# Kernel optimization log

Measured on AMD Instinct MI355X. Metric: run time of the kernel, lower is better.

## Reference

```python
import jax, jax.numpy as jnp
import numpy as np
from jax import lax

B, N, NPOINT, NSAMPLE = 16, 8192, 1024, 32
RADIUS = 0.2
EPS = 1e-5


def setup_inputs() -> dict:
    key = jax.random.key(0)
    ks = jax.random.split(key, 6)
    return {
        "xyz": jax.random.uniform(ks[0], (B, N, 3), dtype=jnp.float32),
        "points": jax.random.normal(ks[1], (B, N, 64), dtype=jnp.float32),
        "w1": jax.random.normal(ks[2], (64, 67), dtype=jnp.float32) * 0.1,
        "b1": jnp.zeros((64,), jnp.float32),
        "g1": jnp.ones((64,), jnp.float32),
        "be1": jnp.zeros((64,), jnp.float32),
        "w2": jax.random.normal(ks[3], (64, 64), dtype=jnp.float32) * 0.1,
        "b2": jnp.zeros((64,), jnp.float32),
        "g2": jnp.ones((64,), jnp.float32),
        "be2": jnp.zeros((64,), jnp.float32),
        "w3": jax.random.normal(ks[4], (128, 64), dtype=jnp.float32) * 0.1,
        "b3": jnp.zeros((128,), jnp.float32),
        "g3": jnp.ones((128,), jnp.float32),
        "be3": jnp.zeros((128,), jnp.float32),
    }


def farthest_point_sample(xyz, npoint):
    # Sequential FPS; deterministic start at index 0 (torch uses a random start).
    b, n, _ = xyz.shape
    batch_ix = jnp.arange(b)

    def step(carry, _):
        distance, farthest = carry
        centroid = xyz[batch_ix, farthest]              # [B,3]
        dist = jnp.sum((xyz - centroid[:, None, :]) ** 2, -1)  # [B,N]
        distance = jnp.minimum(distance, dist)
        return (distance, jnp.argmax(distance, -1).astype(jnp.int32)), farthest

    init = (jnp.full((b, n), 1e10, jnp.float32), jnp.zeros((b,), jnp.int32))
    _, idxs = lax.scan(step, init, None, length=npoint)
    return idxs.T                                        # [B,npoint]


def gather_points(points, idx):
    # points [B,N,C], idx [B,...] -> [B,...,C]
    return jax.vmap(lambda p, i: p[i])(points, idx)


def query_ball_point(radius, nsample, xyz, new_xyz):
    b, n, _ = xyz.shape
    sqrd = jnp.sum((new_xyz[:, :, None, :] - xyz[:, None, :, :]) ** 2, -1)  # [B,S,N]
    gidx = jnp.where(sqrd > radius ** 2, n, jnp.arange(n, dtype=jnp.int32)[None, None, :])
    gidx = jnp.sort(gidx, axis=-1)[:, :, :nsample]       # [B,S,K]
    first = gidx[:, :, :1]
    return jnp.where(gidx == n, first, gidx)


def conv_bn_relu(x, w, b, g, be):
    # x [B,C,S,K]; 1x1 conv == channel matmul, then train-mode BN over (B,S,K).
    y = jnp.einsum("bcsk,oc->bosk", x, w) + b[None, :, None, None]
    mean = jnp.mean(y, axis=(0, 2, 3), keepdims=True)
    var = jnp.mean((y - mean) ** 2, axis=(0, 2, 3), keepdims=True)
    yhat = (y - mean) * lax.rsqrt(var + EPS)
    return jax.nn.relu(yhat * g[None, :, None, None] + be[None, :, None, None])


def reference(xyz, points, w1, b1, g1, be1, w2, b2, g2, be2, w3, b3, g3, be3):
    fps_idx = farthest_point_sample(xyz, NPOINT)          # [B,S]
    new_xyz = gather_points(xyz, fps_idx)                 # [B,S,3]
    idx = query_ball_point(RADIUS, NSAMPLE, xyz, new_xyz) # [B,S,K]
    grouped_xyz = gather_points(xyz, idx)                 # [B,S,K,3]
    grouped_xyz_norm = grouped_xyz - new_xyz[:, :, None, :]
    grouped_points = gather_points(points, idx)           # [B,S,K,64]
    new_points = jnp.concatenate([grouped_xyz_norm, grouped_points], axis=-1)
    x = jnp.transpose(new_points, (0, 3, 1, 2))           # [B,67,S,K]
    x = conv_bn_relu(x, w1, b1, g1, be1)
    x = conv_bn_relu(x, w2, b2, g2, be2)
    x = conv_bn_relu(x, w3, b3, g3, be3)
    new_points_out = jnp.max(x, axis=-1)                  # [B,128,S]
    return new_xyz, new_points_out
```

## Files before the change

kernel.cpp:

```cpp
#include <hip/hip_runtime.h>
#include <hip/hip_bf16.h>

typedef unsigned short u16;
typedef unsigned long long u64;
typedef __attribute__((ext_vector_type(8))) short short8;
typedef __attribute__((ext_vector_type(4))) float f32x4;

#define NN 8192
#define SSAMP 1024
#define KK 32
#define NT_F 524288.0f
#define EPSV 1e-5f

__device__ __forceinline__ u64 umax64(u64 a, u64 b) { return a > b ? a : b; }

template <int C>
__device__ __forceinline__ void dppstep(unsigned& hi, unsigned& lo) {
  unsigned h2 = (unsigned)__builtin_amdgcn_update_dpp(0, (int)hi, C, 0xF, 0xF, true);
  unsigned l2 = (unsigned)__builtin_amdgcn_update_dpp(0, (int)lo, C, 0xF, 0xF, true);
  u64 a = ((u64)hi << 32) | lo;
  u64 b = ((u64)h2 << 32) | l2;
  bool g = b > a;
  hi = g ? h2 : hi;
  lo = g ? l2 : lo;
}

__device__ __forceinline__ u64 wave_max_key(u64 key) {
  unsigned hi = (unsigned)(key >> 32), lo = (unsigned)key;
  dppstep<0x111>(hi, lo);
  dppstep<0x112>(hi, lo);
  dppstep<0x114>(hi, lo);
  dppstep<0x118>(hi, lo);
  dppstep<0x142>(hi, lo);
  dppstep<0x143>(hi, lo);
  return ((u64)hi << 32) | lo;
}

__device__ __forceinline__ int morton3(int ix, int iy, int iz) {
  int m = (((ix >> 0) & 1) << 2) | (((iy >> 0) & 1) << 1) | (((iz >> 0) & 1) << 0);
  m |= (((ix >> 1) & 1) << 5) | (((iy >> 1) & 1) << 4) | (((iz >> 1) & 1) << 3);
  m |= (((ix >> 2) & 1) << 8) | (((iy >> 2) & 1) << 7) | (((iz >> 2) & 1) << 6);
  return m;
}

__global__ __launch_bounds__(1024, 1) void fps_bucket_kernel(const float* __restrict__ xyz,
                                                             float* __restrict__ newxyz) {
  extern __shared__ float dynls[];
  float* sx = dynls;
  float* sy = dynls + NN;
  float* sz = dynls + 2 * NN;
  int* sI = (int*)(dynls + 3 * NN);
  __shared__ int cnt[512], off[512];
  __shared__ u64 candS[3];
  __shared__ int pos0_sh;

  const int b = blockIdx.x, t = threadIdx.x;
  const float* base = xyz + (size_t)b * NN * 3;

  float px[8], py[8], pz[8];
  int pc[8];
  if (t < 512) cnt[t] = 0;
  if (t == 0) { candS[0] = 0; candS[1] = 0; candS[2] = 0; }
  __syncthreads();
#pragma unroll
  for (int j = 0; j < 8; j++) {
    int p = j * 1024 + t;
    px[j] = base[p * 3 + 0];
    py[j] = base[p * 3 + 1];
    pz[j] = base[p * 3 + 2];
    int ix = min(7, (int)(px[j] * 8.0f));
    int iy = min(7, (int)(py[j] * 8.0f));
    int iz = min(7, (int)(pz[j] * 8.0f));
    pc[j] = morton3(ix, iy, iz);
    atomicAdd(&cnt[pc[j]], 1);
  }
  __syncthreads();
  int myc = (t < 512) ? cnt[t] : 0;
  for (int st = 1; st < 512; st <<= 1) {
    int v = 0;
    if (t < 512) { v = cnt[t]; if (t >= st) v += cnt[t - st]; }
    __syncthreads();
    if (t < 512) cnt[t] = v;
    __syncthreads();
  }
  if (t < 512) off[t] = cnt[t] - myc;
  __syncthreads();
#pragma unroll
  for (int j = 0; j < 8; j++) {
    int pos = atomicAdd(&off[pc[j]], 1);
    sx[pos] = px[j]; sy[pos] = py[j]; sz[pos] = pz[j];
    int orig = j * 1024 + t;
    sI[pos] = orig;
    if (orig == 0) pos0_sh = pos;
  }
  __syncthreads();
  float X[8], Y[8], Z[8], D[8];
  unsigned L26[8];
  float lox = 1e30f, loy = 1e30f, loz = 1e30f;
  float hix = -1e30f, hiy = -1e30f, hiz = -1e30f;
#pragma unroll
  for (int j = 0; j < 8; j++) {
    int p = t * 8 + j;
    float x = sx[p], y = sy[p], z = sz[p];
    X[j] = x; Y[j] = y; Z[j] = z; D[j] = 1e10f;
    int orig = sI[p];
    L26[j] = ((unsigned)(8191 - orig) << 13) | (unsigned)p;
    lox = fminf(lox, x); hix = fmaxf(hix, x);
    loy = fminf(loy, y); hiy = fmaxf(hiy, y);
    loz = fminf(loz, z); hiz = fmaxf(hiz, z);
  }
  int cur = pos0_sh;
  u64 ckey = 0;
  float cbd = 1e30f;
  u64 wkeyS = 0;
  int s = 0;

  for (int it = 0; it < SSAMP; it++) {
    const int sn = (s == 2) ? 0 : s + 1;
    float cx = sx[cur], cy = sy[cur], cz = sz[cur];
    if (t == 0) {
      float* o = newxyz + ((size_t)b * SSAMP + it) * 3;
      o[0] = cx; o[1] = cy; o[2] = cz;
    }
    float ddx = fmaxf(fmaxf(lox - cx, cx - hix), 0.f);
    float ddy = fmaxf(fmaxf(loy - cy, cy - hiy), 0.f);
    float ddz = fmaxf(fmaxf(loz - cz, cz - hiz), 0.f);
    float lb2 = fmaf(ddx, ddx, fmaf(ddy, ddy, ddz * ddz));
    bool upd = lb2 <= fmaf(cbd, 1.0001f, 1e-12f);
    if (__ballot(upd)) {
      if (upd) {
        u64 k = 0;
        float bd = -1.0f;
#pragma unroll
        for (int j = 0; j < 8; j++) {
          float dx = __fsub_rn(X[j], cx);
          float dy = __fsub_rn(Y[j], cy);
          float dz = __fsub_rn(Z[j], cz);
          float d = __fadd_rn(__fadd_rn(__fmul_rn(dx, dx), __fmul_rn(dy, dy)), __fmul_rn(dz, dz));
          float dm = fminf(D[j], d);
          D[j] = dm;
          bd = fmaxf(bd, dm);
          u64 kj = ((u64)__float_as_uint(dm) << 26) | (u64)L26[j];
          k = umax64(k, kj);
        }
        ckey = k;
        cbd = bd;
      }
      wkeyS = wave_max_key(ckey);
    }
    if ((t & 63) == 63) atomicMax(&candS[s], wkeyS);
    if (t == 0) candS[sn] = 0;
    __syncthreads();
    cur = (int)(candS[s] & 0x1FFFull);
    s = sn;
  }
}

__global__ __launch_bounds__(512, 1) void fps_fallback_kernel(const float* __restrict__ xyz,
                                                              float* __restrict__ newxyz) {
  const int b = blockIdx.x, t = threadIdx.x;
  const float* base = xyz + (size_t)b * NN * 3;
  __shared__ u64 cand[2][8];
  float X[16], Y[16], Z[16], D[16];
#pragma unroll
  for (int j = 0; j < 16; j++) {
    int p = j * 512 + t;
    X[j] = base[p * 3 + 0];
    Y[j] = base[p * 3 + 1];
    Z[j] = base[p * 3 + 2];
    D[j] = 1e10f;
  }
  __syncthreads();
  int cur = 0;
  const int w = t >> 6;
  for (int it = 0; it < SSAMP; it++) {
    float cx = base[cur * 3 + 0];
    float cy = base[cur * 3 + 1];
    float cz = base[cur * 3 + 2];
    if (t == 0) {
      float* o = newxyz + ((size_t)b * SSAMP + it) * 3;
      o[0] = cx; o[1] = cy; o[2] = cz;
    }
    float bestd = -1.0f;
    int bj = 0;
#pragma unroll
    for (int j = 0; j < 16; j++) {
      float dx = __fsub_rn(X[j], cx);
      float dy = __fsub_rn(Y[j], cy);
      float dz = __fsub_rn(Z[j], cz);
      float d = __fadd_rn(__fadd_rn(__fmul_rn(dx, dx), __fmul_rn(dy, dy)), __fmul_rn(dz, dz));
      float dm = fminf(D[j], d);
      D[j] = dm;
      bool g = dm > bestd;
      bestd = g ? dm : bestd;
      bj = g ? j : bj;
    }
    u64 key = ((u64)__float_as_uint(bestd) << 32) |
              (u64)(unsigned)~(unsigned)(bj * 512 + t);
    key = wave_max_key(key);
    const int s = it & 1;
    if ((t & 63) == 63) cand[s][w] = key;
    __syncthreads();
    u64 c0 = cand[s][0], c1 = cand[s][1], c2 = cand[s][2], c3 = cand[s][3];
    u64 c4 = cand[s][4], c5 = cand[s][5], c6 = cand[s][6], c7 = cand[s][7];
    u64 a0 = umax64(c0, c1), a1 = umax64(c2, c3), a2 = umax64(c4, c5), a3 = umax64(c6, c7);
    u64 best = umax64(umax64(a0, a1), umax64(a2, a3));
    cur = (int)(~(unsigned)(best & 0xFFFFFFFFull));
  }
}

__global__ __launch_bounds__(256) void ballq_kernel(const float* __restrict__ xyz,
                                                    const float* __restrict__ newxyz,
                                                    int* __restrict__ ballidx) {
  const int wid = blockIdx.x * 4 + (threadIdx.x >> 6);
  const int lane = threadIdx.x & 63;
  const int b = wid >> 10;
  const float* base = xyz + (size_t)b * NN * 3;
  const float cx = newxyz[wid * 3 + 0];
  const float cy = newxyz[wid * 3 + 1];
  const float cz = newxyz[wid * 3 + 2];
  int* op = ballidx + (size_t)wid * KK;
  int cnt = 0, first = -1;
  for (int p0 = 0; p0 < NN; p0 += 64) {
    const int p = p0 + lane;
    float dx = __fsub_rn(cx, base[p * 3 + 0]);
    float dy = __fsub_rn(cy, base[p * 3 + 1]);
    float dz = __fsub_rn(cz, base[p * 3 + 2]);
    float d = __fadd_rn(__fadd_rn(__fmul_rn(dx, dx), __fmul_rn(dy, dy)), __fmul_rn(dz, dz));
    bool hit = d <= 0.04f;
    u64 m = __ballot(hit);
    if (m) {
      if (first < 0) first = p0 + __ffsll((long long)m) - 1;
      int rank = __popcll(m & ((1ull << lane) - 1ull));
      int slot = cnt + rank;
      if (hit && slot < KK) op[slot] = p;
      cnt += __popcll(m);
      if (cnt >= KK) break;
    }
  }
  if (cnt < KK && lane >= cnt && lane < KK) op[lane] = first;
}

__global__ __launch_bounds__(256) void collapse_kernel(const float* __restrict__ bkt,
                                                       float* __restrict__ dst) {
  int e = blockIdx.x * 256 + threadIdx.x;
  float s = 0.f;
#pragma unroll 8
  for (int u = 0; u < 64; u++) s += bkt[u * 512 + e];
  dst[e] = s;
}

__device__ __forceinline__ void put2(short8& r, int x, float f0, float f1) {
  __hip_bfloat162 p = __float22bfloat162_rn(make_float2(f0, f1));
  unsigned u = *(const unsigned*)&p;
  r[x] = (short)(u16)(u & 0xFFFF);
  r[x + 1] = (short)(u16)(u >> 16);
}

__device__ __forceinline__ short8 bn_pack8(const u16 h[8], const float* sS, const float* sT, int c0) {
  short8 r;
#pragma unroll
  for (int x = 0; x < 8; x += 2) {
    float f0 = __bfloat162float(*(const __hip_bfloat16*)&h[x]);
    float f1 = __bfloat162float(*(const __hip_bfloat16*)&h[x + 1]);
    f0 = fmaxf(fmaf(f0, sS[c0 + x], sT[c0 + x]), 0.f);
    f1 = fmaxf(fmaf(f1, sS[c0 + x + 1], sT[c0 + x + 1]), 0.f);
    put2(r, x, f0, f1);
  }
  return r;
}

__device__ __forceinline__ short8 w_pack8(const float v[8]) {
  short8 r;
#pragma unroll
  for (int x = 0; x < 8; x += 2) put2(r, x, v[x], v[x + 1]);
  return r;
}

__global__ __launch_bounds__(256) void gemm1_mfma_kernel(const float* __restrict__ xyz,
                                                         const float* __restrict__ pts,
                                                         const float* __restrict__ w1,
                                                         const float* __restrict__ b1,
                                                         const float* __restrict__ newxyz,
                                                         const int* __restrict__ ballidx,
                                                         u16* __restrict__ Y,
                                                         float* __restrict__ bkt) {
  __shared__ __align__(16) short Af[12 * 64 * 8];
  __shared__ __align__(16) short Bf[12 * 64 * 8];
  __shared__ __align__(16) u16 Cs[64 * 72];
  __shared__ int sidx[64];
  __shared__ float snx[6];
  __shared__ float sSum[64], sSq[64];
  const int t = threadIdx.x, blk = blockIdx.x;
  const int pbase = blk * 64;
  const int g0 = pbase >> 5;
  const int b = g0 >> 10;
  if (t < 64) sidx[t] = ballidx[pbase + t];
  if (t < 6) snx[t] = newxyz[(size_t)g0 * 3 + t];
  __syncthreads();
  {
    int r = t >> 2, q = t & 3;
    const float4* prow = (const float4*)(pts + ((size_t)b * NN + sidx[r]) * 64);
    float4 v0 = prow[q * 4 + 0], v1 = prow[q * 4 + 1];
    float4 v2 = prow[q * 4 + 2], v3 = prow[q * 4 + 3];
    float f0[8] = {v0.x, v0.y, v0.z, v0.w, v1.x, v1.y, v1.z, v1.w};
    float f1[8] = {v2.x, v2.y, v2.z, v2.w, v3.x, v3.y, v3.z, v3.w};
    int kt = q >> 1, mt = r >> 4, m = r & 15;
    int qp0 = (2 * q) & 3, qp1 = (2 * q + 1) & 3;
    *(short8*)&Af[((mt * 3 + kt) * 64 + qp0 * 16 + m) * 8] = w_pack8(f0);
    *(short8*)&Af[((mt * 3 + kt) * 64 + qp1 * 16 + m) * 8] = w_pack8(f1);
  }
  {
    int o = t >> 2, q = t & 3;
    const float* wr = w1 + o * 67 + 3 + q * 16;
    float f0[8], f1[8];
#pragma unroll
    for (int x = 0; x < 8; x++) { f0[x] = wr[x]; f1[x] = wr[8 + x]; }
    int kt = q >> 1, nt = o >> 4, n = o & 15;
    int qp0 = (2 * q) & 3, qp1 = (2 * q + 1) & 3;
    *(short8*)&Bf[((nt * 3 + kt) * 64 + qp0 * 16 + n) * 8] = w_pack8(f0);
    *(short8*)&Bf[((nt * 3 + kt) * 64 + qp1 * 16 + n) * 8] = w_pack8(f1);
  }
  if (t < 64) {
    const float* xp = xyz + ((size_t)b * NN + sidx[t]) * 3;
    int g = t >> 5, mt = t >> 4, m = t & 15;
    float xn = xp[0] - snx[g * 3 + 0];
    float yn = xp[1] - snx[g * 3 + 1];
    float zn = xp[2] - snx[g * 3 + 2];
    short8 s0 = {0, 0, 0, 0, 0, 0, 0, 0};
    short8 z8 = {0, 0, 0, 0, 0, 0, 0, 0};
    __hip_bfloat16 hb;
    hb = __float2bfloat16(xn); s0[0] = *(const short*)&hb;
    hb = __float2bfloat16(yn); s0[1] = *(const short*)&hb;
    hb = __float2bfloat16(zn); s0[2] = *(const short*)&hb;
    *(short8*)&Af[((mt * 3 + 2) * 64 + 0 * 16 + m) * 8] = s0;
    *(short8*)&Af[((mt * 3 + 2) * 64 + 1 * 16 + m) * 8] = z8;
    *(short8*)&Af[((mt * 3 + 2) * 64 + 2 * 16 + m) * 8] = z8;
    *(short8*)&Af[((mt * 3 + 2) * 64 + 3 * 16 + m) * 8] = z8;
  } else if (t < 128) {
    int o = t - 64, nt = o >> 4, n = o & 15;
    short8 s0 = {0, 0, 0, 0, 0, 0, 0, 0};
    short8 z8 = {0, 0, 0, 0, 0, 0, 0, 0};
    __hip_bfloat16 hb;
    hb = __float2bfloat16(w1[o * 67 + 0]); s0[0] = *(const short*)&hb;
    hb = __float2bfloat16(w1[o * 67 + 1]); s0[1] = *(const short*)&hb;
    hb = __float2bfloat16(w1[o * 67 + 2]); s0[2] = *(const short*)&hb;
    *(short8*)&Bf[((nt * 3 + 2) * 64 + 0 * 16 + n) * 8] = s0;
    *(short8*)&Bf[((nt * 3 + 2) * 64 + 1 * 16 + n) * 8] = z8;
    *(short8*)&Bf[((nt * 3 + 2) * 64 + 2 * 16 + n) * 8] = z8;
    *(short8*)&Bf[((nt * 3 + 2) * 64 + 3 * 16 + n) * 8] = z8;
  }
  __syncthreads();
  const int w = t >> 6, L = t & 63, q = L >> 4;
  const int nt = w;
  short8 b0 = *(const short8*)&Bf[((nt * 3 + 0) * 64 + L) * 8];
  short8 b1v = *(const short8*)&Bf[((nt * 3 + 1) * 64 + L) * 8];
  short8 b2v = *(const short8*)&Bf[((nt * 3 + 2) * 64 + L) * 8];
  const int o = nt * 16 + (L & 15);
  const float bl = b1[o];
  f32x4 acc[4];
#pragma unroll
  for (int mt = 0; mt < 4; mt++) {
    acc[mt] = (f32x4){0.f, 0.f, 0.f, 0.f};
    short8 a0 = *(const short8*)&Af[((mt * 3 + 0) * 64 + L) * 8];
    short8 a1 = *(const short8*)&Af[((mt * 3 + 1) * 64 + L) * 8];
    short8 a2 = *(const short8*)&Af[((mt * 3 + 2) * 64 + L) * 8];
    acc[mt] = __builtin_amdgcn_mfma_f32_16x16x32_bf16(a0, b0, acc[mt], 0, 0, 0);
    acc[mt] = __builtin_amdgcn_mfma_f32_16x16x32_bf16(a1, b1v, acc[mt], 0, 0, 0);
    acc[mt] = __builtin_amdgcn_mfma_f32_16x16x32_bf16(a2, b2v, acc[mt], 0, 0, 0);
  }
  float s = 0.f, q2 = 0.f;
#pragma unroll
  for (int mt = 0; mt < 4; mt++) {
    float yv[4];
#pragma unroll
    for (int r = 0; r < 4; r++) {
      yv[r] = acc[mt][r] + bl;
      s += yv[r]; q2 += yv[r] * yv[r];
    }
#pragma unroll
    for (int r = 0; r < 4; r += 2) {
      __hip_bfloat162 p = __float22bfloat162_rn(make_float2(yv[r], yv[r + 1]));
      unsigned u = *(const unsigned*)&p;
      Cs[(mt * 16 + q * 4 + r) * 72 + o] = (u16)(u & 0xFFFF);
      Cs[(mt * 16 + q * 4 + r + 1) * 72 + o] = (u16)(u >> 16);
    }
  }
  s += __shfl_xor(s, 16); s += __shfl_xor(s, 32);
  q2 += __shfl_xor(q2, 16); q2 += __shfl_xor(q2, 32);
  if (L < 16) { sSum[o] = s; sSq[o] = q2; }
  __syncthreads();
  {
    int r = t >> 2, qq = t & 3;
    uint4 c0 = *(const uint4*)&Cs[r * 72 + qq * 16];
    uint4 c1 = *(const uint4*)&Cs[r * 72 + qq * 16 + 8];
    uint4* yrow = (uint4*)(Y + (size_t)(pbase + r) * 64);
    yrow[qq * 2] = c0; yrow[qq * 2 + 1] = c1;
  }
  float* bb = bkt + (size_t)(blk & 63) * 512;
  if (t < 64) atomicAdd(&bb[t], sSum[t]);
  else if (t < 128) atomicAdd(&bb[64 + (t - 64)], sSq[t - 64]);
}

__global__ __launch_bounds__(256) void gemm2_mfma_kernel(u16* __restrict__ Y,
                                                         const float* __restrict__ w2,
                                                         const float* __restrict__ b2,
                                                         const float* __restrict__ g1,
                                                         const float* __restrict__ be1,
                                                         const float* __restrict__ statsC,
                                                         float* __restrict__ bkt) {
  __shared__ __align__(16) short Af[8 * 64 * 8];
  __shared__ __align__(16) short Bf[8 * 64 * 8];
  __shared__ __align__(16) u16 Cs[64 * 72];
  __shared__ float sS[64], sT[64];
  __shared__ float sSum[64], sSq[64];
  const int t = threadIdx.x, blk = blockIdx.x;
  const int pbase = blk * 64;
  if (t < 64) {
    float mean = statsC[t] * (1.0f / NT_F);
    float var = statsC[64 + t] * (1.0f / NT_F) - mean * mean;
    float s = g1[t] * rsqrtf(var + EPSV);
    sS[t] = s;
    sT[t] = be1[t] - mean * s;
  }
  __syncthreads();
  {
    int r = t >> 2, q = t & 3;
    const uint4* yrow = (const uint4*)(Y + (size_t)(pbase + r) * 64);
    union { uint4 u; u16 h[8]; } v0, v1;
    v0.u = yrow[q * 2]; v1.u = yrow[q * 2 + 1];
    int c0 = q * 16;
    int kt = c0 >> 5, mt = r >> 4;
    int qp0 = (c0 >> 3) & 3, qp1 = ((c0 + 8) >> 3) & 3;
    *(short8*)&Af[(((mt << 1) | kt) * 64 + qp0 * 16 + (r & 15)) * 8] = bn_pack8(v0.h, sS, sT, c0);
    *(short8*)&Af[(((mt << 1) | kt) * 64 + qp1 * 16 + (r & 15)) * 8] = bn_pack8(v1.h, sS, sT, c0 + 8);
  }
  {
    int o = t >> 2, q = t & 3;
    const float* wrow = w2 + o * 64 + q * 16;
    float f0[8], f1[8];
#pragma unroll
    for (int x = 0; x < 8; x++) { f0[x] = wrow[x]; f1[x] = wrow[8 + x]; }
    int c0 = q * 16;
    int kt = c0 >> 5, nt = o >> 4;
    int qp0 = (c0 >> 3) & 3, qp1 = ((c0 + 8) >> 3) & 3;
    *(short8*)&Bf[(((nt << 1) | kt) * 64 + qp0 * 16 + (o & 15)) * 8] = w_pack8(f0);
    *(short8*)&Bf[(((nt << 1) | kt) * 64 + qp1 * 16 + (o & 15)) * 8] = w_pack8(f1);
  }
  __syncthreads();
  const int w = t >> 6, L = t & 63, q = L >> 4;
  const int nt = w;
  short8 b0 = *(const short8*)&Bf[((nt * 2 + 0) * 64 + L) * 8];
  short8 b1 = *(const short8*)&Bf[((nt * 2 + 1) * 64 + L) * 8];
  const int o = nt * 16 + (L & 15);
  const float bl = b2[o];
  f32x4 acc[4];
#pragma unroll
  for (int mt = 0; mt < 4; mt++) {
    acc[mt] = (f32x4){0.f, 0.f, 0.f, 0.f};
    short8 a0 = *(const short8*)&Af[((mt * 2 + 0) * 64 + L) * 8];
    short8 a1 = *(const short8*)&Af[((mt * 2 + 1) * 64 + L) * 8];
    acc[mt] = __builtin_amdgcn_mfma_f32_16x16x32_bf16(a0, b0, acc[mt], 0, 0, 0);
    acc[mt] = __builtin_amdgcn_mfma_f32_16x16x32_bf16(a1, b1, acc[mt], 0, 0, 0);
  }
  float s = 0.f, q2 = 0.f;
#pragma unroll
  for (int mt = 0; mt < 4; mt++) {
    float yv[4];
#pragma unroll
    for (int r = 0; r < 4; r++) {
      yv[r] = acc[mt][r] + bl;
      s += yv[r]; q2 += yv[r] * yv[r];
    }
#pragma unroll
    for (int r = 0; r < 4; r += 2) {
      __hip_bfloat162 p = __float22bfloat162_rn(make_float2(yv[r], yv[r + 1]));
      unsigned u = *(const unsigned*)&p;
      Cs[(mt * 16 + q * 4 + r) * 72 + o] = (u16)(u & 0xFFFF);
      Cs[(mt * 16 + q * 4 + r + 1) * 72 + o] = (u16)(u >> 16);
    }
  }
  s += __shfl_xor(s, 16); s += __shfl_xor(s, 32);
  q2 += __shfl_xor(q2, 16); q2 += __shfl_xor(q2, 32);
  if (L < 16) { sSum[o] = s; sSq[o] = q2; }
  __syncthreads();
  {
    int r = t >> 2, qq = t & 3;
    uint4 c0 = *(const uint4*)&Cs[r * 72 + qq * 16];
    uint4 c1 = *(const uint4*)&Cs[r * 72 + qq * 16 + 8];
    uint4* yrow = (uint4*)(Y + (size_t)(pbase + r) * 64);
    yrow[qq * 2] = c0; yrow[qq * 2 + 1] = c1;
  }
  float* bb = bkt + (size_t)(blk & 63) * 512;
  if (t < 64) atomicAdd(&bb[128 + t], sSum[t]);
  else if (t < 128) atomicAdd(&bb[192 + (t - 64)], sSq[t - 64]);
}

__global__ __launch_bounds__(256) void conv3max_mfma_kernel(const u16* __restrict__ Y,
                                                            const float* __restrict__ w3,
                                                            const float* __restrict__ b3,
                                                            const float* __restrict__ g2,
                                                            const float* __restrict__ be2,
                                                            const float* __restrict__ statsC,
                                                            float* __restrict__ bkt,
                                                            float* __restrict__ gmax,
                                                            float* __restrict__ gmin) {
  __shared__ __align__(16) short Af[8 * 64 * 8];
  __shared__ __align__(16) short Bf[16 * 64 * 8];
  __shared__ float sS[64], sT[64];
  __shared__ float sSum[128], sSq[128];
  const int t = threadIdx.x, blk = blockIdx.x;
  const int pbase = blk * 64;
  if (t < 64) {
    float mean = statsC[128 + t] * (1.0f / NT_F);
    float var = statsC[192 + t] * (1.0f / NT_F) - mean * mean;
    float s = g2[t] * rsqrtf(var + EPSV);
    sS[t] = s;
    sT[t] = be2[t] - mean * s;
  }
  __syncthreads();
  {
    int r = t >> 2, q = t & 3;
    const uint4* yrow = (const uint4*)(Y + (size_t)(pbase + r) * 64);
    union { uint4 u; u16 h[8]; } v0, v1;
    v0.u = yrow[q * 2]; v1.u = yrow[q * 2 + 1];
    int c0 = q * 16;
    int kt = c0 >> 5, mt = r >> 4;
    int qp0 = (c0 >> 3) & 3, qp1 = ((c0 + 8) >> 3) & 3;
    *(short8*)&Af[(((mt << 1) | kt) * 64 + qp0 * 16 + (r & 15)) * 8] = bn_pack8(v0.h, sS, sT, c0);
    *(short8*)&Af[(((mt << 1) | kt) * 64 + qp1 * 16 + (r & 15)) * 8] = bn_pack8(v1.h, sS, sT, c0 + 8);
  }
  {
    int o = t >> 1, h = t & 1;
    const float* wrow = w3 + o * 64 + h * 32;
    int nt = o >> 4;
#pragma unroll
    for (int g = 0; g < 4; g++) {
      float f[8];
#pragma unroll
      for (int x = 0; x < 8; x++) f[x] = wrow[g * 8 + x];
      *(short8*)&Bf[(((nt << 1) | h) * 64 + g * 16 + (o & 15)) * 8] = w_pack8(f);
    }
  }
  __syncthreads();
  const int w = t >> 6, L = t & 63, q = L >> 4;
  f32x4 acc[2][4];
#pragma unroll
  for (int n = 0; n < 2; n++)
#pragma unroll
    for (int mt = 0; mt < 4; mt++) acc[n][mt] = (f32x4){0.f, 0.f, 0.f, 0.f};
  short8 bfr[2][2];
#pragma unroll
  for (int n = 0; n < 2; n++) {
    int nt = 2 * w + n;
    bfr[n][0] = *(const short8*)&Bf[((nt * 2 + 0) * 64 + L) * 8];
    bfr[n][1] = *(const short8*)&Bf[((nt * 2 + 1) * 64 + L) * 8];
  }
#pragma unroll
  for (int mt = 0; mt < 4; mt++) {
    short8 a0 = *(const short8*)&Af[((mt * 2 + 0) * 64 + L) * 8];
    short8 a1 = *(const short8*)&Af[((mt * 2 + 1) * 64 + L) * 8];
#pragma unroll
    for (int n = 0; n < 2; n++) {
      acc[n][mt] = __builtin_amdgcn_mfma_f32_16x16x32_bf16(a0, bfr[n][0], acc[n][mt], 0, 0, 0);
      acc[n][mt] = __builtin_amdgcn_mfma_f32_16x16x32_bf16(a1, bfr[n][1], acc[n][mt], 0, 0, 0);
    }
  }
#pragma unroll
  for (int n = 0; n < 2; n++) {
    int o = (2 * w + n) * 16 + (L & 15);
    float bl = b3[o];
    float s = 0.f, q2 = 0.f;
    float gmx[2] = {-1e30f, -1e30f}, gmn[2] = {1e30f, 1e30f};
#pragma unroll
    for (int mt = 0; mt < 4; mt++) {
      int g = mt >> 1;
#pragma unroll
      for (int r = 0; r < 4; r++) {
        float y = acc[n][mt][r] + bl;
        s += y; q2 += y * y;
        gmx[g] = fmaxf(gmx[g], y);
        gmn[g] = fminf(gmn[g], y);
      }
    }
    s += __shfl_xor(s, 16); s += __shfl_xor(s, 32);
    q2 += __shfl_xor(q2, 16); q2 += __shfl_xor(q2, 32);
#pragma unroll
    for (int g = 0; g < 2; g++) {
      gmx[g] = fmaxf(gmx[g], __shfl_xor(gmx[g], 16));
      gmx[g] = fmaxf(gmx[g], __shfl_xor(gmx[g], 32));
      gmn[g] = fminf(gmn[g], __shfl_xor(gmn[g], 16));
      gmn[g] = fminf(gmn[g], __shfl_xor(gmn[g], 32));
    }
    if (L < 16) {
      sSum[o] = s; sSq[o] = q2;
#pragma unroll
      for (int g = 0; g < 2; g++) {
        gmax[(size_t)(blk * 2 + g) * 128 + o] = gmx[g];
        gmin[(size_t)(blk * 2 + g) * 128 + o] = gmn[g];
      }
    }
  }
  __syncthreads();
  float* bb = bkt + (size_t)(blk & 63) * 512;
  if (t < 128) atomicAdd(&bb[256 + t], sSum[t]);
  else atomicAdd(&bb[384 + (t - 128)], sSq[t - 128]);
}

__global__ __launch_bounds__(256) void finalize_kernel(const float* __restrict__ gmax,
                                                       const float* __restrict__ gmin,
                                                       const float* __restrict__ statsC,
                                                       const float* __restrict__ g3,
                                                       const float* __restrict__ be3,
                                                       float* __restrict__ outf) {
  __shared__ float smax[64 * 65], smin[64 * 65];
  __shared__ float ssc[64], ssh[64];
  const int t = threadIdx.x, blk = blockIdx.x;
  const int b = blk >> 5, st = (blk >> 1) & 15, oh = blk & 1;
  const int o0 = oh * 64, g0 = b * 1024 + st * 64;
  if (t < 64) {
    int o = o0 + t;
    float mean = statsC[256 + o] * (1.0f / NT_F);
    float var = statsC[384 + o] * (1.0f / NT_F) - mean * mean;
    float sc = g3[o] * rsqrtf(var + EPSV);
    ssc[t] = sc;
    ssh[t] = be3[o] - mean * sc;
  }
  const int col = t & 63, rw = t >> 6;
#pragma unroll
  for (int k = 0; k < 16; k++) {
    int r = k * 4 + rw;
    smax[r * 65 + col] = gmax[(size_t)(g0 + r) * 128 + o0 + col];
    smin[r * 65 + col] = gmin[(size_t)(g0 + r) * 128 + o0 + col];
  }
  __syncthreads();
#pragma unroll
  for (int k = 0; k < 16; k++) {
    int o = k * 4 + rw;
    float sc = ssc[o], sh = ssh[o];
    float v = sc > 0.f ? smax[col * 65 + o] : smin[col * 65 + o];
    outf[((size_t)(b * 128 + o0 + o)) * 1024 + st * 64 + col] = fmaxf(fmaf(v, sc, sh), 0.f);
  }
}

extern "C" void kernel_launch(void* const* d_in, const int* in_sizes, int n_in,
                              void* d_out, int out_size, void* d_ws, size_t ws_size,
                              hipStream_t stream) {
  const float* xyz = (const float*)d_in[0];
  const float* pts = (const float*)d_in[1];
  const float* w1 = (const float*)d_in[2];
  const float* b1 = (const float*)d_in[3];
  const float* g1 = (const float*)d_in[4];
  const float* be1 = (const float*)d_in[5];
  const float* w2 = (const float*)d_in[6];
  const float* b2 = (const float*)d_in[7];
  const float* g2 = (const float*)d_in[8];
  const float* be2 = (const float*)d_in[9];
  const float* w3 = (const float*)d_in[10];
  const float* b3 = (const float*)d_in[11];
  const float* g3 = (const float*)d_in[12];
  const float* be3 = (const float*)d_in[13];

  float* out = (float*)d_out;
  float* newxyz = out;
  float* outfeat = out + 49152;

  char* ws = (char*)d_ws;
  int* ballidx = (int*)ws;
  float* bkt = (float*)(ws + (2 << 20));
  float* statsC = (float*)(ws + (2 << 20) + 131072);
  float* gmax = (float*)(ws + (4 << 20));
  float* gmin = (float*)(ws + (12 << 20));
  u16* Y = (u16*)(ws + (20 << 20));

  hipMemsetAsync(bkt, 0, 64 * 512 * sizeof(float), stream);

  bool use_bucket = false;
  {
    hipError_t e = hipFuncSetAttribute((const void*)fps_bucket_kernel,
                                       hipFuncAttributeMaxDynamicSharedMemorySize, 131072);
    if (e == hipSuccess) {
      int nb = 0;
      hipError_t e2 = hipOccupancyMaxActiveBlocksPerMultiprocessor(
          &nb, (const void*)fps_bucket_kernel, 1024, 131072);
      use_bucket = (e2 == hipSuccess && nb >= 1);
    }
  }
  if (use_bucket)
    fps_bucket_kernel<<<16, 1024, 131072, stream>>>(xyz, newxyz);
  else
    fps_fallback_kernel<<<16, 512, 0, stream>>>(xyz, newxyz);

  ballq_kernel<<<4096, 256, 0, stream>>>(xyz, newxyz, ballidx);
  gemm1_mfma_kernel<<<8192, 256, 0, stream>>>(xyz, pts, w1, b1, newxyz, ballidx, Y, bkt);
  collapse_kernel<<<2, 256, 0, stream>>>(bkt, statsC);
  gemm2_mfma_kernel<<<8192, 256, 0, stream>>>(Y, w2, b2, g1, be1, statsC, bkt);
  collapse_kernel<<<2, 256, 0, stream>>>(bkt, statsC);
  conv3max_mfma_kernel<<<8192, 256, 0, stream>>>(Y, w3, b3, g2, be2, statsC, bkt, gmax, gmin);
  collapse_kernel<<<2, 256, 0, stream>>>(bkt, statsC);
  finalize_kernel<<<512, 256, 0, stream>>>(gmax, gmin, statsC, g3, be3, outfeat);
}
```

Baseline: 1.266 ms.

## Fold BN stat collapse into last-block tickets and speed FPS wave argmax

Removes the three collapse_kernel launches and the memset. Bucket zeroing and ticket reset move into ballq_kernel, and the last block of each GEMM kernel, chosen by an atomic ticket, sums the 64 buckets into statsC. Each GEMM block also pays a threadfence plus an extra barrier. Separately, the FPS bucket kernel now takes a cheaper float-only DPP max over cbd and reads the winning lane's key directly when the max is unique, falling back to the full 64-bit key reduction on ties.

After: 3.872 ms. 3.06x slower.

```diff
diff --git a/kernel.cpp b/kernel.cpp
--- a/kernel.cpp
+++ b/kernel.cpp
@@ -33,6 +33,18 @@
   dppstep<0x118>(hi, lo);
   dppstep<0x142>(hi, lo);
   dppstep<0x143>(hi, lo);
+  return ((u64)hi << 32) | lo;
+}
+
+template <int C>
+__device__ __forceinline__ float maxdpp(float v) {
+  float o = __int_as_float(__builtin_amdgcn_update_dpp(0, __float_as_int(v), C, 0xF, 0xF, true));
+  return fmaxf(v, o);
+}
+
+__device__ __forceinline__ u64 rl64(u64 v, int lane) {
+  unsigned lo = (unsigned)__builtin_amdgcn_readlane((int)(unsigned)v, lane);
+  unsigned hi = (unsigned)__builtin_amdgcn_readlane((int)(unsigned)(v >> 32), lane);
   return ((u64)hi << 32) | lo;
 }
 
@@ -146,7 +158,20 @@
         ckey = k;
         cbd = bd;
       }
-      wkeyS = wave_max_key(ckey);
+      float wmp = cbd;
+      wmp = maxdpp<0x111>(wmp);
+      wmp = maxdpp<0x112>(wmp);
+      wmp = maxdpp<0x114>(wmp);
+      wmp = maxdpp<0x118>(wmp);
+      wmp = maxdpp<0x142>(wmp);
+      wmp = maxdpp<0x143>(wmp);
+      float wm = __int_as_float(__builtin_amdgcn_readlane(__float_as_int(wmp), 63));
+      u64 mask = __ballot(cbd == wm);
+      if (__popcll(mask) == 1) {
+        wkeyS = rl64(ckey, (int)(__ffsll((long long)mask) - 1));
+      } else {
+        wkeyS = rl64(wave_max_key(ckey), 63);
+      }
     }
     if ((t & 63) == 63) atomicMax(&candS[s], wkeyS);
     if (t == 0) candS[sn] = 0;
@@ -211,7 +236,14 @@
 
 __global__ __launch_bounds__(256) void ballq_kernel(const float* __restrict__ xyz,
                                                     const float* __restrict__ newxyz,
-                                                    int* __restrict__ ballidx) {
+                                                    int* __restrict__ ballidx,
+                                                    float* __restrict__ bkt,
+                                                    int* __restrict__ tk) {
+  if (blockIdx.x < 64) {
+    for (int k = threadIdx.x; k < 512; k += 256) bkt[blockIdx.x * 512 + k] = 0.f;
+  } else if (blockIdx.x == 64 && threadIdx.x < 4) {
+    tk[threadIdx.x] = 0;
+  }
   const int wid = blockIdx.x * 4 + (threadIdx.x >> 6);
   const int lane = threadIdx.x & 63;
   const int b = wid >> 10;
@@ -241,13 +273,26 @@
   if (cnt < KK && lane >= cnt && lane < KK) op[lane] = first;
 }
 
-__global__ __launch_bounds__(256) void collapse_kernel(const float* __restrict__ bkt,
-                                                       float* __restrict__ dst) {
-  int e = blockIdx.x * 256 + threadIdx.x;
-  float s = 0.f;
-#pragma unroll 8
-  for (int u = 0; u < 64; u++) s += bkt[u * 512 + e];
-  dst[e] = s;
+__device__ __forceinline__ void collapse_tail(float* __restrict__ bkt,
+                                              float* __restrict__ statsC,
+                                              int* __restrict__ tk, int idx,
+                                              int off, int nstat, int t,
+                                              int nblocks) {
+  __shared__ int last_sh;
+  __threadfence();
+  __syncthreads();
+  if (t == 0) last_sh = (atomicAdd(&tk[idx], 1) == nblocks - 1) ? 1 : 0;
+  __syncthreads();
+  if (last_sh && t < nstat) {
+    float s0 = 0.f, s1 = 0.f, s2 = 0.f, s3 = 0.f;
+    for (int u = 0; u < 64; u += 4) {
+      s0 += atomicAdd(&bkt[(u + 0) * 512 + off + t], 0.0f);
+      s1 += atomicAdd(&bkt[(u + 1) * 512 + off + t], 0.0f);
+      s2 += atomicAdd(&bkt[(u + 2) * 512 + off + t], 0.0f);
+      s3 += atomicAdd(&bkt[(u + 3) * 512 + off + t], 0.0f);
+    }
+    statsC[off + t] = (s0 + s1) + (s2 + s3);
+  }
 }
 
 __device__ __forceinline__ void put2(short8& r, int x, float f0, float f1) {
@@ -284,7 +329,9 @@
                                                          const float* __restrict__ newxyz,
                                                          const int* __restrict__ ballidx,
                                                          u16* __restrict__ Y,
-                                                         float* __restrict__ bkt) {
+                                                         float* __restrict__ bkt,
+                                                         float* __restrict__ statsC,
+                                                         int* __restrict__ tk) {
   __shared__ __align__(16) short Af[12 * 64 * 8];
   __shared__ __align__(16) short Bf[12 * 64 * 8];
   __shared__ __align__(16) u16 Cs[64 * 72];
@@ -400,6 +447,7 @@
   float* bb = bkt + (size_t)(blk & 63) * 512;
   if (t < 64) atomicAdd(&bb[t], sSum[t]);
   else if (t < 128) atomicAdd(&bb[64 + (t - 64)], sSq[t - 64]);
+  collapse_tail(bkt, statsC, tk, 0, 0, 128, t, 8192);
 }
 
 __global__ __launch_bounds__(256) void gemm2_mfma_kernel(u16* __restrict__ Y,
@@ -408,7 +456,9 @@
                                                          const float* __restrict__ g1,
                                                          const float* __restrict__ be1,
                                                          const float* __restrict__ statsC,
-                                                         float* __restrict__ bkt) {
+                                                         float* __restrict__ bkt,
+                                                         float* __restrict__ statsW,
+                                                         int* __restrict__ tk) {
   __shared__ __align__(16) short Af[8 * 64 * 8];
   __shared__ __align__(16) short Bf[8 * 64 * 8];
   __shared__ __align__(16) u16 Cs[64 * 72];
@@ -494,6 +544,7 @@
   float* bb = bkt + (size_t)(blk & 63) * 512;
   if (t < 64) atomicAdd(&bb[128 + t], sSum[t]);
   else if (t < 128) atomicAdd(&bb[192 + (t - 64)], sSq[t - 64]);
+  collapse_tail(bkt, statsW, tk, 1, 128, 128, t, 8192);
 }
 
 __global__ __launch_bounds__(256) void conv3max_mfma_kernel(const u16* __restrict__ Y,
@@ -504,7 +555,9 @@
                                                             const float* __restrict__ statsC,
                                                             float* __restrict__ bkt,
                                                             float* __restrict__ gmax,
-                                                            float* __restrict__ gmin) {
+                                                            float* __restrict__ gmin,
+                                                            float* __restrict__ statsW,
+                                                            int* __restrict__ tk) {
   __shared__ __align__(16) short Af[8 * 64 * 8];
   __shared__ __align__(16) short Bf[16 * 64 * 8];
   __shared__ float sS[64], sT[64];
@@ -605,6 +658,7 @@
   float* bb = bkt + (size_t)(blk & 63) * 512;
   if (t < 128) atomicAdd(&bb[256 + t], sSum[t]);
   else atomicAdd(&bb[384 + (t - 128)], sSq[t - 128]);
+  collapse_tail(bkt, statsW, tk, 2, 256, 256, t, 8192);
 }
 
 __global__ __launch_bounds__(256) void finalize_kernel(const float* __restrict__ gmax,
@@ -669,11 +723,10 @@
   int* ballidx = (int*)ws;
   float* bkt = (float*)(ws + (2 << 20));
   float* statsC = (float*)(ws + (2 << 20) + 131072);
+  int* tickets = (int*)(ws + (2 << 20) + 135168);
   float* gmax = (float*)(ws + (4 << 20));
   float* gmin = (float*)(ws + (12 << 20));
   u16* Y = (u16*)(ws + (20 << 20));
-
-  hipMemsetAsync(bkt, 0, 64 * 512 * sizeof(float), stream);
 
   bool use_bucket = false;
   {
@@ -691,12 +744,11 @@
   else
     fps_fallback_kernel<<<16, 512, 0, stream>>>(xyz, newxyz);
 
-  ballq_kernel<<<4096, 256, 0, stream>>>(xyz, newxyz, ballidx);
-  gemm1_mfma_kernel<<<8192, 256, 0, stream>>>(xyz, pts, w1, b1, newxyz, ballidx, Y, bkt);
-  collapse_kernel<<<2, 256, 0, stream>>>(bkt, statsC);
-  gemm2_mfma_kernel<<<8192, 256, 0, stream>>>(Y, w2, b2, g1, be1, statsC, bkt);
-  collapse_kernel<<<2, 256, 0, stream>>>(bkt, statsC);
-  conv3max_mfma_kernel<<<8192, 256, 0, stream>>>(Y, w3, b3, g2, be2, statsC, bkt, gmax, gmin);
-  collapse_kernel<<<2, 256, 0, stream>>>(bkt, statsC);
+  ballq_kernel<<<4096, 256, 0, stream>>>(xyz, newxyz, ballidx, bkt, tickets);
+  gemm1_mfma_kernel<<<8192, 256, 0, stream>>>(xyz, pts, w1, b1, newxyz, ballidx, Y, bkt,
+                                              statsC, tickets);
+  gemm2_mfma_kernel<<<8192, 256, 0, stream>>>(Y, w2, b2, g1, be1, statsC, bkt, statsC, tickets);
+  conv3max_mfma_kernel<<<8192, 256, 0, stream>>>(Y, w3, b3, g2, be2, statsC, bkt, gmax, gmin,
+                                                 statsC, tickets);
   finalize_kernel<<<512, 256, 0, stream>>>(gmax, gmin, statsC, g3, be3, outfeat);
 }
```
